# Performance work log

Hardware: AMD Instinct MI355X
Metric: run time of the kernel (lower is better)

Reference implementation:

```python
import jax, jax.numpy as jnp
import numpy as np

B, CIN, H, W = 32, 512, 16, 16
COUT, HEADS, SPARSITY = 2048, 8, 7
D = COUT // HEADS  # 256, must equal H*W
N = H * W


def conv1x1(x, w, b):
    # x: [B,C,H,W], w: [O,C], b: [O]
    return jnp.einsum('bchw,oc->bohw', x, w) + b[None, :, None, None]


def setup_inputs() -> dict:
    key = jax.random.key(0)
    ks = jax.random.split(key, 11)
    def lin(k, o, c):
        bound = 1.0 / np.sqrt(c)
        kw, kb = jax.random.split(k)
        return (jax.random.uniform(kw, (o, c), jnp.float32, -bound, bound),
                jax.random.uniform(kb, (o,), jnp.float32, -bound, bound))
    Wq, bq = lin(ks[0], COUT, CIN)
    Wk, bk = lin(ks[1], COUT, CIN)
    Wv, bv = lin(ks[2], COUT, CIN)
    Wo, bo = lin(ks[3], COUT, COUT)
    # kaiming_uniform_ on [COUT, COUT]
    gain = np.sqrt(2.0) / np.sqrt(5.0)  # default a=sqrt(5)
    bound = gain * np.sqrt(3.0 / COUT)
    coeff = jax.random.uniform(ks[4], (COUT, COUT), jnp.float32, -bound, bound)
    scale = jnp.array([np.sqrt(D)], jnp.float32)
    x = jax.random.normal(ks[5], (B, CIN, H, W), jnp.float32)
    return {"x": x, "Wq": Wq, "bq": bq, "Wk": Wk, "bk": bk, "Wv": Wv,
            "bv": bv, "Wo": Wo, "bo": bo, "coeff": coeff, "scale": scale}


def reference(x, Wq, bq, Wk, bk, Wv, bv, Wo, bo, coeff, scale):
    # enforce_sparsity: keep top-`SPARSITY` |coeff| per row, zero the rest
    _, idx = jax.lax.top_k(jnp.abs(coeff), SPARSITY)  # [COUT, SPARSITY]
    mask = jnp.zeros(coeff.shape, bool).at[jnp.arange(COUT)[:, None], idx].set(True)
    coeff_s = jnp.where(mask, coeff, 0.0)

    q = conv1x1(x, Wq, bq).reshape(B, HEADS, D, N)
    k = conv1x1(x, Wk, bk).reshape(B, HEADS, D, N)
    v = conv1x1(x, Wv, bv).reshape(B, HEADS, D, N)

    attn = jnp.einsum('bhdn,bhdm->bhnm', q, k) / scale[0]  # [B,h,N,N]
    sparse_attn = jnp.einsum('bhnm,mp->bhnp', attn, coeff_s[:D, :D])
    sparse_attn = jax.nn.softmax(sparse_attn, axis=-1)
    out = jnp.einsum('bhnm,bhmd->bhnd', sparse_attn, v.transpose(0, 1, 3, 2))
    out = out.transpose(0, 1, 3, 2).reshape(B, COUT, H, W)
    return conv1x1(out, Wo, bo)
```

## Files before the change

kernel.cpp:

```cpp
#include <hip/hip_runtime.h>

typedef unsigned short ushort;
typedef __attribute__((ext_vector_type(8))) short short8;
typedef __attribute__((ext_vector_type(8))) unsigned short ushort8;
typedef __attribute__((ext_vector_type(4))) unsigned short ushort4v;
typedef __attribute__((ext_vector_type(4))) float fx4;

#define MAXNNZ (256*7)

__device__ __forceinline__ ushort f2bf(float f) {
    union { float f; unsigned u; } v; v.f = f;
    unsigned r = v.u + 0x7fffu + ((v.u >> 16) & 1u);
    return (ushort)(r >> 16);
}

__device__ __forceinline__ float bf2f(ushort b) {
    union { unsigned u; float f; } v; v.u = ((unsigned)b) << 16;
    return v.f;
}

__device__ __forceinline__ void gload_lds16(const ushort* g, ushort* l) {
    __builtin_amdgcn_global_load_lds(
        (const __attribute__((address_space(1))) unsigned int*)g,
        (__attribute__((address_space(3))) unsigned int*)l, 16, 0, 0);
}

__global__ __launch_bounds__(256)
void topk_kernel(const float* __restrict__ coeff,
                 int* __restrict__ coo_cnt, int* __restrict__ coo_m,
                 int* __restrict__ coo_p, float* __restrict__ coo_v)
{
    int row = blockIdx.x;
    int tid = threadIdx.x;
    const float* crow = coeff + (long)row * 2048;
    float av[8];
#pragma unroll
    for (int i = 0; i < 8; ++i) av[i] = fabsf(crow[tid + 256 * i]);
    __shared__ unsigned long long red[256];
    for (int t = 0; t < 7; ++t) {
        float mx = -1.f; int mi = 0;
#pragma unroll
        for (int i = 0; i < 8; ++i) if (av[i] > mx) { mx = av[i]; mi = i; }
        unsigned col = (unsigned)(tid + 256 * mi);
        unsigned long long pk = ((unsigned long long)__float_as_uint(mx) << 32)
                              | (unsigned long long)(2048u - col);
        red[tid] = pk; __syncthreads();
        for (int s = 128; s > 0; s >>= 1) {
            if (tid < s) { if (red[tid + s] > red[tid]) red[tid] = red[tid + s]; }
            __syncthreads();
        }
        unsigned long long w = red[0];
        __syncthreads();
        unsigned wcol = 2048u - (unsigned)(w & 0xffffffffu);
        if ((wcol & 255u) == (unsigned)tid) av[wcol >> 8] = -1.f;
        if (tid == 0 && wcol < 256u) {
            int pos = atomicAdd(coo_cnt, 1);
            coo_m[pos] = row; coo_p[pos] = (int)wcol; coo_v[pos] = crow[wcol];
        }
    }
}

__global__ __launch_bounds__(256)
void csc_kernel(const int* __restrict__ coo_cnt, const int* __restrict__ coo_m,
                const int* __restrict__ coo_p, const float* __restrict__ coo_v,
                int* __restrict__ csc_ptr, int* __restrict__ csc_m, float* __restrict__ csc_v)
{
    __shared__ int cnt[256];
    __shared__ int off[257];
    __shared__ int cur[256];
    int tid = threadIdx.x;
    cnt[tid] = 0;
    __syncthreads();
    int n = *coo_cnt; if (n > MAXNNZ) n = MAXNNZ;
    for (int e = tid; e < n; e += 256) atomicAdd(&cnt[coo_p[e]], 1);
    __syncthreads();
    if (tid == 0) {
        int s = 0;
        for (int p = 0; p < 256; ++p) { off[p] = s; s += cnt[p]; }
        off[256] = s;
    }
    __syncthreads();
    csc_ptr[tid] = off[tid];
    if (tid == 0) csc_ptr[256] = off[256];
    cur[tid] = off[tid];
    __syncthreads();
    for (int e = tid; e < n; e += 256) {
        int p = coo_p[e];
        int pos = atomicAdd(&cur[p], 1);
        csc_m[pos] = coo_m[e];
        csc_v[pos] = coo_v[e];
    }
}

__global__ void cvt4_kernel(const float* a0, ushort* d0, int n0,
                            const float* a1, ushort* d1, int n1,
                            const float* a2, ushort* d2, int n2,
                            const float* a3, ushort* d3, int n3)
{
    const float* s; ushort* d; int n;
    switch (blockIdx.y) {
        case 0: s = a0; d = d0; n = n0; break;
        case 1: s = a1; d = d1; n = n1; break;
        case 2: s = a2; d = d2; n = n2; break;
        default: s = a3; d = d3; n = n3; break;
    }
    int nv = n >> 2;
    for (int i = blockIdx.x * blockDim.x + threadIdx.x; i < nv; i += gridDim.x * blockDim.x) {
        fx4 v = ((const fx4*)s)[i];
        ushort4v o;
        o[0] = f2bf(v[0]); o[1] = f2bf(v[1]); o[2] = f2bf(v[2]); o[3] = f2bf(v[3]);
        ((ushort4v*)d)[i] = o;
    }
}

__global__ __launch_bounds__(256)
void transpose_f32_bf16(const float* __restrict__ in, ushort* __restrict__ out, int R, int C)
{
    int z = blockIdx.z;
    const float* ib = in + (long)z * R * C;
    ushort* ob = out + (long)z * R * C;
    __shared__ ushort tile[64][72];
    int r0 = blockIdx.x * 64, c0 = blockIdx.y * 64;
    int tid = threadIdx.x;
    int rl = tid >> 2, sg = tid & 3;
#pragma unroll
    for (int h = 0; h < 4; ++h) {
        fx4 v = *(const fx4*)(ib + (long)(r0 + rl) * C + c0 + h * 16 + sg * 4);
#pragma unroll
        for (int i = 0; i < 4; ++i) tile[h * 16 + sg * 4 + i][rl] = f2bf(v[i]);
    }
    __syncthreads();
    int cl = rl;
#pragma unroll
    for (int h = 0; h < 2; ++h) {
        ushort8 vv = *(const ushort8*)(&tile[cl][h * 32 + sg * 8]);
        *(ushort8*)(ob + (long)(c0 + cl) * R + r0 + h * 32 + sg * 8) = vv;
    }
}

__global__ __launch_bounds__(256)
void kcomb_kernel(const ushort* __restrict__ kbT, ushort* __restrict__ ktc,
                  const int* __restrict__ csc_ptr, const int* __restrict__ csc_m,
                  const float* __restrict__ csc_v)
{
    int z = blockIdx.y;
    int tid = threadIdx.x;
    int p = blockIdx.x * 64 + (tid >> 2);
    int d0 = (tid & 3) * 64;
    const ushort* src = kbT + (long)z * 65536;
    float acc[64];
#pragma unroll
    for (int i = 0; i < 64; ++i) acc[i] = 0.f;
    int e0 = csc_ptr[p], e1 = csc_ptr[p + 1];
    for (int e = e0; e < e1; ++e) {
        const ushort* row = src + csc_m[e] * 256 + d0;
        float c = csc_v[e];
#pragma unroll
        for (int u = 0; u < 8; ++u) {
            ushort8 v = *(const ushort8*)(row + u * 8);
#pragma unroll
            for (int t = 0; t < 8; ++t) acc[u * 8 + t] += bf2f(v[t]) * c;
        }
    }
    ushort* dst = ktc + (long)z * 65536 + (long)p * 256 + d0;
#pragma unroll
    for (int u = 0; u < 8; ++u) {
        ushort8 o;
#pragma unroll
        for (int t = 0; t < 8; ++t) o[t] = f2bf(acc[u * 8 + t]);
        *(ushort8*)(dst + u * 8) = o;
    }
}

template<int MODE>
__global__ __launch_bounds__(256)
void gemm128(const ushort* __restrict__ A, long long strideA,
             const ushort* __restrict__ B, long long strideB,
             void* __restrict__ C,
             const float* __restrict__ bias0, const float* __restrict__ bias1,
             const float* __restrict__ bias2,
             int N, int K)
{
    int z = blockIdx.z;
    const ushort* Ab = A + (long long)z * strideA;
    const ushort* Bb = B + (long long)z * strideB;
    int m0 = blockIdx.x * 128, n0 = blockIdx.y * 128;

    __shared__ __align__(16) ushort As[128 * 32];
    __shared__ __align__(16) ushort Bs[128 * 32];
    __shared__ __align__(16) ushort Ct[(MODE == 3 || MODE == 4) ? 128 * 136 : 8];

    int tid = threadIdx.x;
    int wave = tid >> 6, lane = tid & 63;
    int wrow = wave >> 1, wcol = wave & 1;
    int l16 = lane & 15, quad = lane >> 4;
    int lrow = lane >> 2, lkq = lane & 3;

    fx4 acc[4][4];
#pragma unroll
    for (int i = 0; i < 4; ++i)
#pragma unroll
        for (int j = 0; j < 4; ++j) acc[i][j] = (fx4){0.f, 0.f, 0.f, 0.f};

    const ushort* gA0 = Ab + (long)(m0 + wave * 16 + lrow) * K + lkq * 8;
    const ushort* gA1 = gA0 + (long)64 * K;
    const ushort* gB0 = Bb + (long)(n0 + wave * 16 + lrow) * K + lkq * 8;
    const ushort* gB1 = gB0 + (long)64 * K;
    ushort* lA0 = As + (wave * 16) * 32;
    ushort* lA1 = As + (64 + wave * 16) * 32;
    ushort* lB0 = Bs + (wave * 16) * 32;
    ushort* lB1 = Bs + (64 + wave * 16) * 32;

    for (int kc = 0; kc < K; kc += 32) {
        __syncthreads();
        gload_lds16(gA0 + kc, lA0);
        gload_lds16(gA1 + kc, lA1);
        gload_lds16(gB0 + kc, lB0);
        gload_lds16(gB1 + kc, lB1);
        __syncthreads();

        short8 af[4], bf[4];
#pragma unroll
        for (int i = 0; i < 4; ++i)
            af[i] = *(const short8*)(As + (wrow * 64 + i * 16 + l16) * 32 + quad * 8);
#pragma unroll
        for (int j = 0; j < 4; ++j)
            bf[j] = *(const short8*)(Bs + (wcol * 64 + j * 16 + l16) * 32 + quad * 8);
#pragma unroll
        for (int i = 0; i < 4; ++i)
#pragma unroll
            for (int j = 0; j < 4; ++j)
                acc[i][j] = __builtin_amdgcn_mfma_f32_16x16x32_bf16(af[i], bf[j], acc[i][j], 0, 0, 0);
    }

    if (MODE == 5) {
#pragma unroll
        for (int i = 0; i < 4; ++i)
#pragma unroll
            for (int j = 0; j < 4; ++j)
#pragma unroll
                for (int r2 = 0; r2 < 4; ++r2) {
                    int m = m0 + wrow * 64 + i * 16 + quad * 4 + r2;
                    int n2 = n0 + wcol * 64 + j * 16 + l16;
                    int zb = n2 >> 8, n = n2 & 255;
                    ((float*)C)[(long long)zb * 524288 + (long)m * 256 + n]
                        = acc[i][j][r2] + bias0[m];
                }
        return;
    }

    if (MODE == 3) {
#pragma unroll
        for (int i = 0; i < 4; ++i)
#pragma unroll
            for (int j = 0; j < 4; ++j) {
                int ml = wrow * 64 + i * 16 + quad * 4;
                int nl = wcol * 64 + j * 16 + l16;
                ushort4v pk;
#pragma unroll
                for (int r = 0; r < 4; ++r) pk[r] = f2bf(acc[i][j][r]);
                *(ushort4v*)(Ct + nl * 136 + ml) = pk;
            }
        __syncthreads();
        long long zb = z >> 3; int zh = z & 7;
        int nl = tid >> 3, mc = (tid & 7) * 16;
#pragma unroll
        for (int p4 = 0; p4 < 4; ++p4) {
            int n = p4 * 32 + nl;
            ushort8 v0 = *(const ushort8*)(Ct + n * 136 + mc);
            ushort8 v1 = *(const ushort8*)(Ct + n * 136 + mc + 8);
            ushort* dst = (ushort*)C + zb * 524288 + (long)(n0 + n) * 2048
                        + zh * 256 + m0 + mc;
            *(ushort8*)dst = v0;
            *(ushort8*)(dst + 8) = v1;
        }
        return;
    }

    if (MODE == 4) {
        int sec = m0 >> 11;
        int ms0 = m0 & 2047;
        int zb = n0 >> 8, nlo = n0 & 255;
        if (sec < 2) {
            const float* bs = (sec == 0) ? bias0 : bias1;
#pragma unroll
            for (int i = 0; i < 4; ++i)
#pragma unroll
                for (int j = 0; j < 4; ++j) {
                    int ml = wrow * 64 + i * 16 + quad * 4;
                    int nl = wcol * 64 + j * 16 + l16;
                    ushort4v pk;
#pragma unroll
                    for (int r = 0; r < 4; ++r)
                        pk[r] = f2bf(acc[i][j][r] + bs[ms0 + ml + r]);
                    *(ushort4v*)(Ct + nl * 136 + ml) = pk;
                }
            __syncthreads();
            int h = ms0 >> 8, d0 = m0 & 255;
            int nl = tid >> 3, mc = (tid & 7) * 16;
            ushort* base = (ushort*)C + (long long)sec * 16777216
                         + (long long)zb * 524288 + (long)h * 65536;
#pragma unroll
            for (int p4 = 0; p4 < 4; ++p4) {
                int n = p4 * 32 + nl;
                ushort8 v0 = *(const ushort8*)(Ct + n * 136 + mc);
                ushort8 v1 = *(const ushort8*)(Ct + n * 136 + mc + 8);
                ushort* dst = base + (long)(nlo + n) * 256 + d0 + mc;
                *(ushort8*)dst = v0;
                *(ushort8*)(dst + 8) = v1;
            }
        } else {
#pragma unroll
            for (int i = 0; i < 4; ++i)
#pragma unroll
                for (int j = 0; j < 4; ++j) {
                    int ml = wrow * 64 + i * 16 + quad * 4;
                    int nl = wcol * 64 + j * 16 + l16;
#pragma unroll
                    for (int r = 0; r < 4; ++r)
                        Ct[(ml + r) * 136 + nl] = f2bf(acc[i][j][r] + bias2[ms0 + ml + r]);
                }
            __syncthreads();
            int ml = tid >> 3, nc = (tid & 7) * 16;
            ushort* base = (ushort*)C + 33554432LL + (long long)zb * 524288;
#pragma unroll
            for (int p4 = 0; p4 < 4; ++p4) {
                int m = p4 * 32 + ml;
                ushort8 v0 = *(const ushort8*)(Ct + m * 136 + nc);
                ushort8 v1 = *(const ushort8*)(Ct + m * 136 + nc + 8);
                ushort* dst = base + (long)(ms0 + m) * 256 + nlo + nc;
                *(ushort8*)dst = v0;
                *(ushort8*)(dst + 8) = v1;
            }
        }
        return;
    }
}

__global__ __launch_bounds__(256)
void tsm_kernel(const ushort* __restrict__ Q, const ushort* __restrict__ Kt,
                ushort* __restrict__ P, const float* __restrict__ scale_src)
{
    int z = blockIdx.y;
    const ushort* Ab = Q + (long)z * 65536;
    const ushort* Bb = Kt + (long)z * 65536;
    int n0 = blockIdx.x * 128;

    __shared__ __align__(16) ushort As[128 * 32];
    __shared__ __align__(16) ushort Bs[256 * 32];
    __shared__ float rmax[2][128];
    __shared__ float rsum[2][128];

    int tid = threadIdx.x;
    int wave = tid >> 6, lane = tid & 63;
    int wrow = wave >> 1, wcol = wave & 1;
    int l16 = lane & 15, quad = lane >> 4;
    int lrow = lane >> 2, lkq = lane & 3;

    fx4 acc[4][8];
#pragma unroll
    for (int i = 0; i < 4; ++i)
#pragma unroll
        for (int j = 0; j < 8; ++j) acc[i][j] = (fx4){0.f, 0.f, 0.f, 0.f};

    const ushort* gA0 = Ab + (long)(n0 + wave * 16 + lrow) * 256 + lkq * 8;
    const ushort* gA1 = gA0 + 64 * 256;
    const ushort* gB0 = Bb + (long)(wave * 16 + lrow) * 256 + lkq * 8;
    ushort* lA0 = As + (wave * 16) * 32;
    ushort* lA1 = As + (64 + wave * 16) * 32;
    ushort* lB0 = Bs + (wave * 16) * 32;

    for (int kc = 0; kc < 256; kc += 32) {
        __syncthreads();
        gload_lds16(gA0 + kc, lA0);
        gload_lds16(gA1 + kc, lA1);
        gload_lds16(gB0 + kc, lB0);
        gload_lds16(gB0 + 64 * 256 + kc, lB0 + 64 * 32);
        gload_lds16(gB0 + 128 * 256 + kc, lB0 + 128 * 32);
        gload_lds16(gB0 + 192 * 256 + kc, lB0 + 192 * 32);
        __syncthreads();

        short8 af[4], bf[8];
#pragma unroll
        for (int i = 0; i < 4; ++i)
            af[i] = *(const short8*)(As + (wrow * 64 + i * 16 + l16) * 32 + quad * 8);
#pragma unroll
        for (int j = 0; j < 8; ++j)
            bf[j] = *(const short8*)(Bs + (wcol * 128 + j * 16 + l16) * 32 + quad * 8);
#pragma unroll
        for (int i = 0; i < 4; ++i)
#pragma unroll
            for (int j = 0; j < 8; ++j)
                acc[i][j] = __builtin_amdgcn_mfma_f32_16x16x32_bf16(af[i], bf[j], acc[i][j], 0, 0, 0);
    }

    float sc = 1.0f / scale_src[0];
#pragma unroll
    for (int i = 0; i < 4; ++i)
#pragma unroll
        for (int j = 0; j < 8; ++j)
#pragma unroll
            for (int r = 0; r < 4; ++r) acc[i][j][r] *= sc;

    float lm[4][4];
#pragma unroll
    for (int i = 0; i < 4; ++i)
#pragma unroll
        for (int r = 0; r < 4; ++r) {
            float m = -1e30f;
#pragma unroll
            for (int j = 0; j < 8; ++j) m = fmaxf(m, acc[i][j][r]);
            lm[i][r] = m;
        }
#pragma unroll
    for (int d = 1; d < 16; d <<= 1)
#pragma unroll
        for (int i = 0; i < 4; ++i)
#pragma unroll
            for (int r = 0; r < 4; ++r) lm[i][r] = fmaxf(lm[i][r], __shfl_xor(lm[i][r], d, 16));
    if (l16 == 0) {
#pragma unroll
        for (int i = 0; i < 4; ++i)
#pragma unroll
            for (int r = 0; r < 4; ++r)
                rmax[wcol][wrow * 64 + i * 16 + quad * 4 + r] = lm[i][r];
    }
    __syncthreads();

    float ls[4][4];
#pragma unroll
    for (int i = 0; i < 4; ++i)
#pragma unroll
        for (int r = 0; r < 4; ++r) {
            int row = wrow * 64 + i * 16 + quad * 4 + r;
            float M = fmaxf(rmax[0][row], rmax[1][row]);
            float s = 0.f;
#pragma unroll
            for (int j = 0; j < 8; ++j) {
                float e = __expf(acc[i][j][r] - M);
                acc[i][j][r] = e;
                s += e;
            }
            ls[i][r] = s;
        }
#pragma unroll
    for (int d = 1; d < 16; d <<= 1)
#pragma unroll
        for (int i = 0; i < 4; ++i)
#pragma unroll
            for (int r = 0; r < 4; ++r) ls[i][r] += __shfl_xor(ls[i][r], d, 16);
    if (l16 == 0) {
#pragma unroll
        for (int i = 0; i < 4; ++i)
#pragma unroll
            for (int r = 0; r < 4; ++r)
                rsum[wcol][wrow * 64 + i * 16 + quad * 4 + r] = ls[i][r];
    }
    __syncthreads();

    ushort* Pb = P + (long)z * 65536;
#pragma unroll
    for (int i = 0; i < 4; ++i)
#pragma unroll
        for (int r = 0; r < 4; ++r) {
            int row = wrow * 64 + i * 16 + quad * 4 + r;
            float inv = 1.0f / (rsum[0][row] + rsum[1][row]);
#pragma unroll
            for (int j = 0; j < 8; ++j)
                Pb[(long)(n0 + row) * 256 + wcol * 128 + j * 16 + l16] = f2bf(acc[i][j][r] * inv);
        }
}

extern "C" void kernel_launch(void* const* d_in, const int* in_sizes, int n_in,
                              void* d_out, int out_size, void* d_ws, size_t ws_size,
                              hipStream_t stream)
{
    const float* x     = (const float*)d_in[0];
    const float* Wq    = (const float*)d_in[1];
    const float* bq    = (const float*)d_in[2];
    const float* Wk    = (const float*)d_in[3];
    const float* bk    = (const float*)d_in[4];
    const float* Wv    = (const float*)d_in[5];
    const float* bv    = (const float*)d_in[6];
    const float* Wo    = (const float*)d_in[7];
    const float* bo    = (const float*)d_in[8];
    const float* coeff = (const float*)d_in[9];
    const float* scale = (const float*)d_in[10];
    float* out = (float*)d_out;

    size_t o = 0;
    char* w = (char*)d_ws;
    auto take = [&](size_t bytes) -> void* {
        void* p = w + o; o += (bytes + 255) & ~(size_t)255; return p;
    };
    int*    coo_cnt = (int*)take(4);
    int*    coo_m   = (int*)take(MAXNNZ * 4);
    int*    coo_p   = (int*)take(MAXNNZ * 4);
    float*  coo_v   = (float*)take(MAXNNZ * 4);
    int*    csc_ptr = (int*)take(257 * 4);
    int*    csc_m   = (int*)take(MAXNNZ * 4);
    float*  csc_v   = (float*)take(MAXNNZ * 4);
    ushort* wqkv = (ushort*)take(6144L * 512 * 2);
    ushort* wob  = (ushort*)take(2048L * 2048 * 2);
    ushort* xT   = (ushort*)take(32L * 256 * 512 * 2);
    ushort* qkv  = (ushort*)take(3 * 16777216L * 2);
    ushort* qbT = qkv;
    ushort* kbT = qkv + 16777216L;
    ushort* vb  = qkv + 33554432L;
    ushort* ktc = (ushort*)take(16777216L * 2);
    ushort* P_ws = kbT;
    ushort* obT  = qbT;
    (void)in_sizes; (void)n_in; (void)out_size; (void)ws_size;

    hipMemsetAsync(coo_cnt, 0, 4, stream);
    topk_kernel<<<256, 256, 0, stream>>>(coeff, coo_cnt, coo_m, coo_p, coo_v);
    csc_kernel<<<1, 256, 0, stream>>>(coo_cnt, coo_m, coo_p, coo_v, csc_ptr, csc_m, csc_v);

    cvt4_kernel<<<dim3(1024, 4, 1), 256, 0, stream>>>(
        Wq, wqkv, 2048 * 512, Wk, wqkv + 2048L * 512, 2048 * 512,
        Wv, wqkv + 4096L * 512, 2048 * 512, Wo, wob, 2048 * 2048);
    transpose_f32_bf16<<<dim3(8, 4, 32), 256, 0, stream>>>(x, xT, 512, 256);

    gemm128<4><<<dim3(48, 64, 1), 256, 0, stream>>>(
        wqkv, 0, xT, 0, qkv, bq, bk, bv, 8192, 512);

    kcomb_kernel<<<dim3(4, 256), 256, 0, stream>>>(kbT, ktc, csc_ptr, csc_m, csc_v);

    tsm_kernel<<<dim3(2, 256), 256, 0, stream>>>(qbT, ktc, P_ws, scale);

    gemm128<3><<<dim3(2, 2, 256), 256, 0, stream>>>(
        vb, 65536, P_ws, 65536, obT, nullptr, nullptr, nullptr, 256, 256);

    gemm128<5><<<dim3(16, 64, 1), 256, 0, stream>>>(
        wob, 0, obT, 0, out, bo, nullptr, nullptr, 8192, 2048);
}
```

Measured before the change: 431.1 us.

## Add 256x256-tile pipelined GEMM with XCD swizzle for QKV and output projections

Adds a new gemm256 kernel with 512 threads, 256x256 output tiles and a 4-stage global-to-LDS pipeline gated by explicit vmcnt waits and barriers. It also remaps block IDs across XCDs for better L2 locality and raises MFMA wave priority. The kernel replaces gemm128 for the QKV projection (mode 4) and the output projection (mode 5), aiming for more data reuse per tile and better hiding of load latency. In exchange it uses much more LDS and more registers, which lowers occupancy, and the epilogue reuses the staging LDS in two halves.

```diff
diff --git a/kernel.cpp b/kernel.cpp
--- a/kernel.cpp
+++ b/kernel.cpp
@@ -188,7 +188,7 @@
 
     __shared__ __align__(16) ushort As[128 * 32];
     __shared__ __align__(16) ushort Bs[128 * 32];
-    __shared__ __align__(16) ushort Ct[(MODE == 3 || MODE == 4) ? 128 * 136 : 8];
+    __shared__ __align__(16) ushort Ct[(MODE == 3) ? 128 * 136 : 8];
 
     int tid = threadIdx.x;
     int wave = tid >> 6, lane = tid & 63;
@@ -233,22 +233,6 @@
                 acc[i][j] = __builtin_amdgcn_mfma_f32_16x16x32_bf16(af[i], bf[j], acc[i][j], 0, 0, 0);
     }
 
-    if (MODE == 5) {
-#pragma unroll
-        for (int i = 0; i < 4; ++i)
-#pragma unroll
-            for (int j = 0; j < 4; ++j)
-#pragma unroll
-                for (int r2 = 0; r2 < 4; ++r2) {
-                    int m = m0 + wrow * 64 + i * 16 + quad * 4 + r2;
-                    int n2 = n0 + wcol * 64 + j * 16 + l16;
-                    int zb = n2 >> 8, n = n2 & 255;
-                    ((float*)C)[(long long)zb * 524288 + (long)m * 256 + n]
-                        = acc[i][j][r2] + bias0[m];
-                }
-        return;
-    }
-
     if (MODE == 3) {
 #pragma unroll
         for (int i = 0; i < 4; ++i)
@@ -276,61 +260,171 @@
         }
         return;
     }
+}
+
+template<int MODE>
+__global__ __launch_bounds__(512, 2)
+void gemm256(const ushort* __restrict__ A, const ushort* __restrict__ B,
+             void* __restrict__ C,
+             const float* __restrict__ bias0, const float* __restrict__ bias1,
+             const float* __restrict__ bias2,
+             int MT, int K)
+{
+    __shared__ __align__(16) ushort lds[4][2][8192];
+
+    int nwg = gridDim.x;
+    int bid = blockIdx.x;
+    int cpx = nwg >> 3;
+    int swz = (bid & 7) * cpx + (bid >> 3);
+    int mt = swz % MT, nt = swz / MT;
+    int m0 = mt << 8, n0 = nt << 8;
+
+    int tid = threadIdx.x;
+    int wave = tid >> 6, lane = tid & 63;
+    int wr = wave >> 2, wc = wave & 3;
+    int l16 = lane & 15, quad = lane >> 4;
+
+    const ushort* gA0 = A + (long long)(m0 + wave * 16 + (lane >> 2)) * K + (lane & 3) * 8;
+    const ushort* gA1 = gA0 + (long long)128 * K;
+    const ushort* gB0 = B + (long long)(n0 + wave * 16 + (lane >> 2)) * K + (lane & 3) * 8;
+    const ushort* gB1 = gB0 + (long long)128 * K;
+    int ldso = wave * 512;
+
+    fx4 acc[8][4];
+#pragma unroll
+    for (int i = 0; i < 8; ++i)
+#pragma unroll
+        for (int j = 0; j < 4; ++j) acc[i][j] = (fx4){0.f, 0.f, 0.f, 0.f};
+
+    auto stage = [&](int b, int kc) {
+        gload_lds16(gA0 + kc, &lds[b][0][ldso]);
+        gload_lds16(gA1 + kc, &lds[b][0][4096 + ldso]);
+        gload_lds16(gB0 + kc, &lds[b][1][ldso]);
+        gload_lds16(gB1 + kc, &lds[b][1][4096 + ldso]);
+    };
+    auto compute = [&](int b) {
+        short8 af[8], bf[4];
+#pragma unroll
+        for (int i = 0; i < 8; ++i)
+            af[i] = *(const short8*)(&lds[b][0][(wr * 128 + i * 16 + l16) * 32 + quad * 8]);
+#pragma unroll
+        for (int j = 0; j < 4; ++j)
+            bf[j] = *(const short8*)(&lds[b][1][(wc * 64 + j * 16 + l16) * 32 + quad * 8]);
+        __builtin_amdgcn_s_setprio(1);
+#pragma unroll
+        for (int i = 0; i < 8; ++i)
+#pragma unroll
+            for (int j = 0; j < 4; ++j)
+                acc[i][j] = __builtin_amdgcn_mfma_f32_16x16x32_bf16(af[i], bf[j], acc[i][j], 0, 0, 0);
+        __builtin_amdgcn_s_setprio(0);
+    };
+
+    int NT = K >> 5;
+    stage(0, 0); stage(1, 32); stage(2, 64);
+    int kt = 0;
+    for (; kt + 3 < NT; ++kt) {
+        stage((kt + 3) & 3, (kt + 3) << 5);
+        asm volatile("s_waitcnt vmcnt(12)" ::: "memory");
+        __builtin_amdgcn_s_barrier();
+        asm volatile("" ::: "memory");
+        compute(kt & 3);
+        asm volatile("" ::: "memory");
+        __builtin_amdgcn_s_barrier();
+    }
+    asm volatile("s_waitcnt vmcnt(8)" ::: "memory");
+    __builtin_amdgcn_s_barrier();
+    asm volatile("" ::: "memory");
+    compute(kt & 3); ++kt;
+    asm volatile("" ::: "memory");
+    __builtin_amdgcn_s_barrier();
+    asm volatile("s_waitcnt vmcnt(4)" ::: "memory");
+    __builtin_amdgcn_s_barrier();
+    asm volatile("" ::: "memory");
+    compute(kt & 3); ++kt;
+    asm volatile("" ::: "memory");
+    __builtin_amdgcn_s_barrier();
+    asm volatile("s_waitcnt vmcnt(0)" ::: "memory");
+    __builtin_amdgcn_s_barrier();
+    asm volatile("" ::: "memory");
+    compute(kt & 3);
+    __builtin_amdgcn_s_barrier();
+
+    if (MODE == 5) {
+        float* Cf = (float*)C + (long long)nt * 524288;
+#pragma unroll
+        for (int i = 0; i < 8; ++i) {
+            int m = m0 + wr * 128 + i * 16 + quad * 4;
+#pragma unroll
+            for (int j = 0; j < 4; ++j) {
+                int n = wc * 64 + j * 16 + l16;
+                float* dst = Cf + (long long)m * 256 + n;
+#pragma unroll
+                for (int r = 0; r < 4; ++r)
+                    dst[(long)r * 256] = acc[i][j][r] + bias0[m + r];
+            }
+        }
+        return;
+    }
 
     if (MODE == 4) {
         int sec = m0 >> 11;
         int ms0 = m0 & 2047;
-        int zb = n0 >> 8, nlo = n0 & 255;
+        ushort* ct = &lds[0][0][0];
         if (sec < 2) {
             const float* bs = (sec == 0) ? bias0 : bias1;
-#pragma unroll
-            for (int i = 0; i < 4; ++i)
-#pragma unroll
-                for (int j = 0; j < 4; ++j) {
-                    int ml = wrow * 64 + i * 16 + quad * 4;
-                    int nl = wcol * 64 + j * 16 + l16;
-                    ushort4v pk;
-#pragma unroll
-                    for (int r = 0; r < 4; ++r)
-                        pk[r] = f2bf(acc[i][j][r] + bs[ms0 + ml + r]);
-                    *(ushort4v*)(Ct + nl * 136 + ml) = pk;
+            ushort* base = (ushort*)C + (long long)sec * 16777216
+                         + (long long)nt * 524288 + (long long)(ms0 >> 8) * 65536;
+#pragma unroll
+            for (int hh = 0; hh < 2; ++hh) {
+                if ((wc >> 1) == hh) {
+#pragma unroll
+                    for (int i = 0; i < 8; ++i)
+#pragma unroll
+                        for (int j = 0; j < 4; ++j) {
+                            int nl = (wc & 1) * 64 + j * 16 + l16;
+                            int ml = wr * 128 + i * 16 + quad * 4;
+                            ushort4v pk;
+#pragma unroll
+                            for (int r = 0; r < 4; ++r)
+                                pk[r] = f2bf(acc[i][j][r] + bs[ms0 + ml + r]);
+                            *(ushort4v*)(ct + nl * 264 + ml) = pk;
+                        }
                 }
-            __syncthreads();
-            int h = ms0 >> 8, d0 = m0 & 255;
-            int nl = tid >> 3, mc = (tid & 7) * 16;
-            ushort* base = (ushort*)C + (long long)sec * 16777216
-                         + (long long)zb * 524288 + (long)h * 65536;
-#pragma unroll
-            for (int p4 = 0; p4 < 4; ++p4) {
-                int n = p4 * 32 + nl;
-                ushort8 v0 = *(const ushort8*)(Ct + n * 136 + mc);
-                ushort8 v1 = *(const ushort8*)(Ct + n * 136 + mc + 8);
-                ushort* dst = base + (long)(nlo + n) * 256 + d0 + mc;
-                *(ushort8*)dst = v0;
-                *(ushort8*)(dst + 8) = v1;
+                __syncthreads();
+                int row = tid & 127, c0 = (tid >> 7) * 64;
+                ushort* dst = base + (long long)(hh * 128 + row) * 256 + c0;
+                const ushort* src = ct + row * 264 + c0;
+#pragma unroll
+                for (int u = 0; u < 8; ++u)
+                    *(ushort8*)(dst + u * 8) = *(const ushort8*)(src + u * 8);
+                __syncthreads();
             }
         } else {
-#pragma unroll
-            for (int i = 0; i < 4; ++i)
-#pragma unroll
-                for (int j = 0; j < 4; ++j) {
-                    int ml = wrow * 64 + i * 16 + quad * 4;
-                    int nl = wcol * 64 + j * 16 + l16;
-#pragma unroll
-                    for (int r = 0; r < 4; ++r)
-                        Ct[(ml + r) * 136 + nl] = f2bf(acc[i][j][r] + bias2[ms0 + ml + r]);
+            ushort* base = (ushort*)C + 33554432LL + (long long)nt * 524288
+                         + (long long)ms0 * 256;
+#pragma unroll
+            for (int hh = 0; hh < 2; ++hh) {
+                if (wr == hh) {
+#pragma unroll
+                    for (int i = 0; i < 8; ++i)
+#pragma unroll
+                        for (int j = 0; j < 4; ++j) {
+                            int nl = wc * 64 + j * 16 + l16;
+                            int ml = i * 16 + quad * 4;
+#pragma unroll
+                            for (int r = 0; r < 4; ++r)
+                                ct[(ml + r) * 264 + nl] =
+                                    f2bf(acc[i][j][r] + bias2[ms0 + hh * 128 + ml + r]);
+                        }
                 }
-            __syncthreads();
-            int ml = tid >> 3, nc = (tid & 7) * 16;
-            ushort* base = (ushort*)C + 33554432LL + (long long)zb * 524288;
-#pragma unroll
-            for (int p4 = 0; p4 < 4; ++p4) {
-                int m = p4 * 32 + ml;
-                ushort8 v0 = *(const ushort8*)(Ct + m * 136 + nc);
-                ushort8 v1 = *(const ushort8*)(Ct + m * 136 + nc + 8);
-                ushort* dst = base + (long)(ms0 + m) * 256 + nlo + nc;
-                *(ushort8*)dst = v0;
-                *(ushort8*)(dst + 8) = v1;
+                __syncthreads();
+                int row = tid & 127, c0 = (tid >> 7) * 64;
+                ushort* dst = base + (long long)(hh * 128 + row) * 256 + c0;
+                const ushort* src = ct + row * 264 + c0;
+#pragma unroll
+                for (int u = 0; u < 8; ++u)
+                    *(ushort8*)(dst + u * 8) = *(const ushort8*)(src + u * 8);
+                __syncthreads();
             }
         }
         return;
@@ -521,8 +615,8 @@
         Wv, wqkv + 4096L * 512, 2048 * 512, Wo, wob, 2048 * 2048);
     transpose_f32_bf16<<<dim3(8, 4, 32), 256, 0, stream>>>(x, xT, 512, 256);
 
-    gemm128<4><<<dim3(48, 64, 1), 256, 0, stream>>>(
-        wqkv, 0, xT, 0, qkv, bq, bk, bv, 8192, 512);
+    gemm256<4><<<dim3(768, 1, 1), dim3(512, 1, 1), 0, stream>>>(
+        wqkv, xT, qkv, bq, bk, bv, 24, 512);
 
     kcomb_kernel<<<dim3(4, 256), 256, 0, stream>>>(kbT, ktc, csc_ptr, csc_m, csc_v);
 
@@ -531,6 +625,6 @@
     gemm128<3><<<dim3(2, 2, 256), 256, 0, stream>>>(
         vb, 65536, P_ws, 65536, obT, nullptr, nullptr, nullptr, 256, 256);
 
-    gemm128<5><<<dim3(16, 64, 1), 256, 0, stream>>>(
-        wob, 0, obT, 0, out, bo, nullptr, nullptr, 8192, 2048);
-}
+    gemm256<5><<<dim3(256, 1, 1), dim3(512, 1, 1), 0, stream>>>(
+        wob, obT, out, bo, nullptr, nullptr, 8, 2048);
+}
```

Measured after the change: 397.7 us. 1.08x faster.
